# Kernel tuning notes

Hardware: AMD Instinct MI355X
Metric: run time of the kernel (lower is better)

## Reference

```python
import jax, jax.numpy as jnp
import numpy as np

HEADS = 16
DIM_HEAD = 64
SCALE = DIM_HEAD ** -0.5


def setup_inputs() -> dict:
    key = jax.random.key(0)
    ks = jax.random.split(key, 6)
    B, Nq, Nkv, D = 2, 512, 4096, 1024
    inner = HEADS * DIM_HEAD  # 1024
    s = 1.0 / np.sqrt(D)
    return {
        "q": jax.random.normal(ks[0], (B, Nq, D), jnp.float32),
        "kv": jax.random.normal(ks[1], (B, Nkv, D), jnp.float32),
        "mask": jnp.ones((B, Nkv), dtype=bool),
        "Wq": jax.random.normal(ks[2], (D, inner), jnp.float32) * s,
        "Wkv": jax.random.normal(ks[3], (D, 2 * inner), jnp.float32) * s,
        "Wo": jax.random.normal(ks[4], (inner, D), jnp.float32) * (1.0 / np.sqrt(inner)),
        "bo": jnp.zeros((D,), jnp.float32),
    }


def reference(q, kv, mask, Wq, Wkv, Wo, bo):
    B, Nq, D = q.shape
    Nkv = kv.shape[1]
    h, dh = HEADS, DIM_HEAD
    # projections
    qh = (q @ Wq).reshape(B, Nq, h, dh).transpose(0, 2, 1, 3)        # (B,h,Nq,dh)
    kvp = kv @ Wkv                                                    # (B,Nkv,2*inner)
    k, v = jnp.split(kvp, 2, axis=-1)
    kh = k.reshape(B, Nkv, h, dh).transpose(0, 2, 1, 3)              # (B,h,Nkv,dh)
    vh = v.reshape(B, Nkv, h, dh).transpose(0, 2, 1, 3)
    # scaled dot-product cross-attention
    attn = jnp.einsum("bhqd,bhkd->bhqk", qh, kh) * SCALE             # (B,h,Nq,Nkv)
    neg_inf = jnp.finfo(attn.dtype).min
    attn = jnp.where(mask[:, None, None, :], attn, neg_inf)
    attn = jax.nn.softmax(attn, axis=-1)
    out = jnp.einsum("bhqk,bhkd->bhqd", attn, vh)                    # (B,h,Nq,dh)
    out = out.transpose(0, 2, 1, 3).reshape(B, Nq, h * dh)
    return out @ Wo + bo
```

## Files before the change

### kernel.cpp

```cpp
#include <hip/hip_runtime.h>
#include <string.h>
#include <math.h>

typedef unsigned short u16;
typedef __bf16 bf16x8 __attribute__((ext_vector_type(8)));
typedef float floatx4 __attribute__((ext_vector_type(4)));

#define HEADS  16
#define DH     64
#define BATCH  2
#define NQ     512
#define NKV    4096
#define DMODEL 1024
#define INNER  1024
#define SCALE  0.125f
#define LOG2E  1.4426950408889634f
#define FM     12.0f
#define SPLIT  4
#define KEYS_PER_PART (NKV / SPLIT)
#define CH (KEYS_PER_PART / 64)

__device__ __forceinline__ u16 f2bf(float f) {
  union { __bf16 h; u16 u; } v; v.h = (__bf16)f; return v.u;
}

__device__ __forceinline__ void gll16(const u16* g, u16* l) {
  __builtin_amdgcn_global_load_lds(
      (const __attribute__((address_space(1))) unsigned int*)g,
      (__attribute__((address_space(3))) unsigned int*)l, 16, 0, 0);
}

__global__ __launch_bounds__(256) void prep(const float* __restrict__ q,
                                            const float* __restrict__ kv,
                                            const float* __restrict__ Wq,
                                            const float* __restrict__ Wkv,
                                            const float* __restrict__ Wo,
                                            u16* __restrict__ qb,
                                            u16* __restrict__ kvb,
                                            u16* __restrict__ Wqt,
                                            u16* __restrict__ Wkvt,
                                            u16* __restrict__ Wot) {
  __shared__ float tile[32][33];
  const int bx = blockIdx.x, tid = threadIdx.x;
  if (bx < 4608) {
    const float* x; u16* y; size_t i;
    if (bx < 512) { x = q;  y = qb;  i = (size_t)bx * 256 + tid; }
    else          { x = kv; y = kvb; i = (size_t)(bx - 512) * 256 + tid; }
    const float4* p = (const float4*)x + i * 2;
    float4 a = p[0], b = p[1];
    union { u16 s[8]; uint4 v; } o;
    o.s[0] = f2bf(a.x); o.s[1] = f2bf(a.y); o.s[2] = f2bf(a.z); o.s[3] = f2bf(a.w);
    o.s[4] = f2bf(b.x); o.s[5] = f2bf(b.y); o.s[6] = f2bf(b.z); o.s[7] = f2bf(b.w);
    *(uint4*)(y + i * 8) = o.v;
    return;
  }
  const float* W; u16* Wt; int K, N, n0, k0, t;
  if (bx < 5632)      { t = bx - 4608; W = Wq;  Wt = Wqt;  K = 1024; N = 1024; n0 = (t & 31) * 32; k0 = (t >> 5) * 32; }
  else if (bx < 7680) { t = bx - 5632; W = Wkv; Wt = Wkvt; K = 1024; N = 2048; n0 = (t & 63) * 32; k0 = (t >> 6) * 32; }
  else                { t = bx - 7680; W = Wo;  Wt = Wot;  K = 1024; N = 1024; n0 = (t & 31) * 32; k0 = (t >> 5) * 32; }
  const int tx = tid & 31, ty = tid >> 5;
  for (int i = 0; i < 32; i += 8)
    tile[ty + i][tx] = W[(size_t)(k0 + ty + i) * N + n0 + tx];
  __syncthreads();
  for (int i = 0; i < 32; i += 8)
    Wt[(size_t)(n0 + ty + i) * K + k0 + tx] = f2bf(tile[tx][ty + i]);
}

__global__ __launch_bounds__(256) void gemm_kv(const u16* __restrict__ A,
                                               const u16* __restrict__ Bt,
                                               u16* __restrict__ Kb,
                                               u16* __restrict__ Vb) {
  const int K = DMODEL;
  __shared__ __align__(16) u16 As[128 * 32];
  __shared__ __align__(16) u16 Bs[128 * 32];
  const int tid  = threadIdx.x;
  const int lane = tid & 63, wave = tid >> 6;
  const int wr = wave >> 1, wc = wave & 1;
  const int l16 = lane & 15, quad = lane >> 4;
  const int bm = blockIdx.y, bn = blockIdx.x;
  const int r0 = tid >> 2;
  const int kb = (tid & 3) ^ ((tid >> 3) & 3);
  const u16* aP0 = A  + ((size_t)bm * 128 + r0)      * K + kb * 8;
  const u16* aP1 = A  + ((size_t)bm * 128 + r0 + 64) * K + kb * 8;
  const u16* bP0 = Bt + ((size_t)bn * 128 + r0)      * K + kb * 8;
  const u16* bP1 = Bt + ((size_t)bn * 128 + r0 + 64) * K + kb * 8;
  u16* ldsA0 = As + wave * 512;
  u16* ldsA1 = As + 2048 + wave * 512;
  u16* ldsB0 = Bs + wave * 512;
  u16* ldsB1 = Bs + 2048 + wave * 512;
  const int ko = ((quad ^ ((l16 >> 1) & 3)) << 3);

  floatx4 acc[4][4] = {};
  for (int k0 = 0; k0 < K; k0 += 32) {
    gll16(aP0 + k0, ldsA0);
    gll16(aP1 + k0, ldsA1);
    gll16(bP0 + k0, ldsB0);
    gll16(bP1 + k0, ldsB1);
    __syncthreads();
    bf16x8 af[4], bfr[4];
#pragma unroll
    for (int i = 0; i < 4; ++i)
      af[i] = *(const bf16x8*)&As[(wr * 64 + i * 16 + l16) * 32 + ko];
#pragma unroll
    for (int j = 0; j < 4; ++j)
      bfr[j] = *(const bf16x8*)&Bs[(wc * 64 + j * 16 + l16) * 32 + ko];
#pragma unroll
    for (int i = 0; i < 4; ++i)
#pragma unroll
      for (int j = 0; j < 4; ++j)
        acc[i][j] = __builtin_amdgcn_mfma_f32_16x16x32_bf16(af[i], bfr[j], acc[i][j], 0, 0, 0);
    __syncthreads();
  }
  u16* Cb = (bn < 8) ? Kb : Vb;
  const int colbase = ((bn < 8) ? bn : bn - 8) * 128;
#pragma unroll
  for (int i = 0; i < 4; ++i) {
    const int rowb = bm * 128 + wr * 64 + i * 16 + quad * 4;
#pragma unroll
    for (int j = 0; j < 4; ++j) {
      const int col = colbase + wc * 64 + j * 16 + l16;
#pragma unroll
      for (int r = 0; r < 4; ++r)
        Cb[(size_t)(rowb + r) * 1024 + col] = f2bf(acc[i][j][r]);
    }
  }
}

template<bool OUT_BF16>
__global__ __launch_bounds__(256) void gemm64(const u16* __restrict__ A,
                                              const u16* __restrict__ Bt,
                                              float* __restrict__ Cf,
                                              u16* __restrict__ Cb,
                                              const float* __restrict__ bias,
                                              int M, int N, int K) {
  __shared__ __align__(16) u16 As[64 * 64];
  __shared__ __align__(16) u16 Bs[64 * 64];
  const int tid = threadIdx.x;
  const int lane = tid & 63, wave = tid >> 6;
  const int wr = wave >> 1, wc = wave & 1;
  const int l16 = lane & 15, quad = lane >> 4;
  const int bm = blockIdx.y, bn = blockIdx.x;
  const int r0 = tid >> 3;
  const int kbs = (tid & 7) ^ (r0 & 7);
  const u16* aP0 = A  + ((size_t)bm * 64 + r0)      * K + kbs * 8;
  const u16* aP1 = A  + ((size_t)bm * 64 + r0 + 32) * K + kbs * 8;
  const u16* bP0 = Bt + ((size_t)bn * 64 + r0)      * K + kbs * 8;
  const u16* bP1 = Bt + ((size_t)bn * 64 + r0 + 32) * K + kbs * 8;
  u16* ldsA0 = As + wave * 512;
  u16* ldsA1 = As + 2048 + wave * 512;
  u16* ldsB0 = Bs + wave * 512;
  u16* ldsB1 = Bs + 2048 + wave * 512;

  floatx4 acc[2][2] = {};
  for (int k0 = 0; k0 < K; k0 += 64) {
    gll16(aP0 + k0, ldsA0);
    gll16(aP1 + k0, ldsA1);
    gll16(bP0 + k0, ldsB0);
    gll16(bP1 + k0, ldsB1);
    __syncthreads();
    bf16x8 af[2][2], bfr[2][2];
#pragma unroll
    for (int i = 0; i < 2; ++i)
#pragma unroll
      for (int kk = 0; kk < 2; ++kk)
        af[i][kk] = *(const bf16x8*)&As[(wr * 32 + i * 16 + l16) * 64 +
                                        (((kk * 4 + quad) ^ (l16 & 7)) << 3)];
#pragma unroll
    for (int j = 0; j < 2; ++j)
#pragma unroll
      for (int kk = 0; kk < 2; ++kk)
        bfr[j][kk] = *(const bf16x8*)&Bs[(wc * 32 + j * 16 + l16) * 64 +
                                         (((kk * 4 + quad) ^ (l16 & 7)) << 3)];
#pragma unroll
    for (int i = 0; i < 2; ++i)
#pragma unroll
      for (int j = 0; j < 2; ++j) {
        acc[i][j] = __builtin_amdgcn_mfma_f32_16x16x32_bf16(af[i][0], bfr[j][0], acc[i][j], 0, 0, 0);
        acc[i][j] = __builtin_amdgcn_mfma_f32_16x16x32_bf16(af[i][1], bfr[j][1], acc[i][j], 0, 0, 0);
      }
    __syncthreads();
  }
#pragma unroll
  for (int i = 0; i < 2; ++i) {
    const int rowb = bm * 64 + wr * 32 + i * 16 + quad * 4;
#pragma unroll
    for (int j = 0; j < 2; ++j) {
      const int col = bn * 64 + wc * 32 + j * 16 + l16;
#pragma unroll
      for (int r = 0; r < 4; ++r) {
        const size_t idx = (size_t)(rowb + r) * N + col;
        if (OUT_BF16) Cb[idx] = f2bf(acc[i][j][r]);
        else          Cf[idx] = acc[i][j][r] + bias[col];
      }
    }
  }
}

__global__ __launch_bounds__(256) void vtrans(const u16* __restrict__ Vb,
                                              u16* __restrict__ vT) {
  __shared__ u16 t[64 * 72];
  const int bx = blockIdx.x, tid = threadIdx.x;
  const int bh = bx >> 6, tb = bx & 63;
  const int b = bh >> 4, h = bh & 15;
  const int r = tid >> 2, cg = (tid & 3) * 16;
  const u16* src = Vb + ((size_t)(b * NKV + tb * 64 + r)) * 1024 + h * 64 + cg;
  *(uint4*)&t[r * 72 + cg]     = ((const uint4*)src)[0];
  *(uint4*)&t[r * 72 + cg + 8] = ((const uint4*)src)[1];
  __syncthreads();
  const int d = tid >> 2, tg = (tid & 3) * 16;
  union { u16 s[16]; uint4 v[2]; } o;
#pragma unroll
  for (int i = 0; i < 16; ++i) o.s[i] = t[(tg + i) * 72 + d];
  u16* dst = vT + ((size_t)(bh * 64 + d)) * NKV + tb * 64 + tg;
  *(uint4*)dst = o.v[0]; *(uint4*)(dst + 8) = o.v[1];
}

__global__ __launch_bounds__(256) void attn_part(const u16* __restrict__ Qh,
                                                 const u16* __restrict__ Kb,
                                                 const u16* __restrict__ vT,
                                                 const int* __restrict__ mask,
                                                 float* __restrict__ Opart,
                                                 float* __restrict__ Mst,
                                                 float* __restrict__ Lst) {
  __shared__ __align__(16) u16 Ks[64 * 64];
  __shared__ __align__(16) u16 Vs[2][64 * 64];
  __shared__ __align__(16) u16 QP[4608];
  __shared__ float Msk[64];
  const int tid = threadIdx.x;
  const int lane = tid & 63, w = tid >> 6;
  const int l16 = lane & 15, quad = lane >> 4;
  const int part = blockIdx.x & (SPLIT - 1);
  const int qt = (blockIdx.x >> 2) & 7;
  const int h  = (blockIdx.x >> 5) & 15;
  const int b  = blockIdx.x >> 9;
  const int rs = tid >> 2, d0 = (tid & 3) * 16;
  u16* Ps = QP + w * 1152;

  const int r8 = lane >> 3;
  const int kb8 = (lane & 7) ^ (r8 & 7);
  const int key00 = part * KEYS_PER_PART;
  const u16* kSrc = Kb + ((size_t)(b * NKV + key00 + w * 8 + r8)) * 1024 + h * DH + kb8 * 8;
  const u16* vSrc = vT + ((size_t)((b * 16 + h) * 64 + w * 8 + r8)) * NKV + key00 + kb8 * 8;
  u16* ldsK0 = Ks + w * 512;
  u16* ldsK1 = Ks + 2048 + w * 512;
  const int koA = (quad ^ (l16 & 7)) << 3;
  const int koB = ((quad + 4) ^ (l16 & 7)) << 3;

  bf16x8 bones;
  {
    union { u16 s[8]; bf16x8 v; } t1;
    const u16 o1 = (l16 == 0) ? (u16)0x3F80 : (u16)0;
#pragma unroll
    for (int i = 0; i < 8; ++i) t1.s[i] = o1;
    bones = t1.v;
  }

  {
    const uint4* p = (const uint4*)(Qh + ((size_t)(b * NQ + qt * 64 + rs)) * INNER + h * DH + d0);
    *(uint4*)&QP[rs * 72 + d0]     = p[0];
    *(uint4*)&QP[rs * 72 + d0 + 8] = p[1];
  }
  gll16(kSrc, ldsK0);
  gll16(kSrc + 32768, ldsK1);
  gll16(vSrc, Vs[0] + w * 512);
  gll16(vSrc + (size_t)32 * NKV, Vs[0] + 2048 + w * 512);
  float mk0 = 0.f;
  if (tid < 64) mk0 = (mask[(size_t)b * NKV + key00 + tid] != 0) ? -FM : -1e30f;
  __syncthreads();
  bf16x8 aq0 = *(const bf16x8*)&QP[(w * 16 + l16) * 72 + quad * 8];
  bf16x8 aq1 = *(const bf16x8*)&QP[(w * 16 + l16) * 72 + 32 + quad * 8];
  if (tid < 64) Msk[tid] = mk0;
  __syncthreads();

  floatx4 o[4] = {};
  floatx4 lacc = {0.f, 0.f, 0.f, 0.f};
  const float SC = SCALE * LOG2E;

  for (int c = 0; c < CH; ++c) {
    const u16* Vcur = Vs[c & 1];
#pragma unroll
    for (int nt = 0; nt < 4; ++nt) {
      bf16x8 b0 = *(const bf16x8*)&Ks[(nt * 16 + l16) * 64 + koA];
      bf16x8 b1 = *(const bf16x8*)&Ks[(nt * 16 + l16) * 64 + koB];
      floatx4 t = {0.f, 0.f, 0.f, 0.f};
      t = __builtin_amdgcn_mfma_f32_16x16x32_bf16(aq0, b0, t, 0, 0, 0);
      t = __builtin_amdgcn_mfma_f32_16x16x32_bf16(aq1, b1, t, 0, 0, 0);
      const float mk = Msk[nt * 16 + l16];
#pragma unroll
      for (int r = 0; r < 4; ++r)
        Ps[(quad * 4 + r) * 72 + nt * 16 + l16] = f2bf(exp2f(t[r] * SC + mk));
    }
    __syncthreads();
    if (c + 1 < CH) {
      gll16(kSrc + (size_t)(c + 1) * 65536, ldsK0);
      gll16(kSrc + (size_t)(c + 1) * 65536 + 32768, ldsK1);
      u16* vdst = Vs[(c + 1) & 1];
      gll16(vSrc + (c + 1) * 64, vdst + w * 512);
      gll16(vSrc + (c + 1) * 64 + (size_t)32 * NKV, vdst + 2048 + w * 512);
      if (tid < 64)
        Msk[tid] = (mask[(size_t)b * NKV + key00 + (c + 1) * 64 + tid] != 0) ? -FM : -1e30f;
    }
    bf16x8 ap0 = *(const bf16x8*)&Ps[l16 * 72 + quad * 8];
    bf16x8 ap1 = *(const bf16x8*)&Ps[l16 * 72 + 32 + quad * 8];
    lacc = __builtin_amdgcn_mfma_f32_16x16x32_bf16(ap0, bones, lacc, 0, 0, 0);
    lacc = __builtin_amdgcn_mfma_f32_16x16x32_bf16(ap1, bones, lacc, 0, 0, 0);
#pragma unroll
    for (int dt = 0; dt < 4; ++dt) {
      bf16x8 bv0 = *(const bf16x8*)&Vcur[(dt * 16 + l16) * 64 + koA];
      bf16x8 bv1 = *(const bf16x8*)&Vcur[(dt * 16 + l16) * 64 + koB];
      o[dt] = __builtin_amdgcn_mfma_f32_16x16x32_bf16(ap0, bv0, o[dt], 0, 0, 0);
      o[dt] = __builtin_amdgcn_mfma_f32_16x16x32_bf16(ap1, bv1, o[dt], 0, 0, 0);
    }
    __syncthreads();
  }
  const int pid = blockIdx.x;
#pragma unroll
  for (int r = 0; r < 4; ++r) {
    const int q = w * 16 + quad * 4 + r;
    if (l16 == 0) { Mst[pid * 64 + q] = FM; Lst[pid * 64 + q] = lacc[r]; }
#pragma unroll
    for (int dt = 0; dt < 4; ++dt)
      Opart[(size_t)pid * 4096 + q * 64 + dt * 16 + l16] = o[dt][r];
  }
}

__global__ __launch_bounds__(256) void attn_combine(const float* __restrict__ Opart,
                                                    const float* __restrict__ Mst,
                                                    const float* __restrict__ Lst,
                                                    u16* __restrict__ Out) {
  const int x = blockIdx.x;
  const int t = threadIdx.x;
  const int q = t >> 2, db = (t & 3) * 16;
  const int b = x >> 7, h = (x >> 3) & 15, qt = x & 7;
  float ms[SPLIT], ls[SPLIT];
#pragma unroll
  for (int s = 0; s < SPLIT; ++s) {
    ms[s] = Mst[(size_t)(x * SPLIT + s) * 64 + q];
    ls[s] = Lst[(size_t)(x * SPLIT + s) * 64 + q];
  }
  float M = fmaxf(fmaxf(ms[0], ms[1]), fmaxf(ms[2], ms[3]));
  float wgt[SPLIT], L = 0.f;
#pragma unroll
  for (int s = 0; s < SPLIT; ++s) { wgt[s] = exp2f(ms[s] - M); L += wgt[s] * ls[s]; }
  const float inv = 1.0f / L;
  float acc[16] = {};
#pragma unroll
  for (int s = 0; s < SPLIT; ++s) {
    const float4* p = (const float4*)&Opart[(size_t)(x * SPLIT + s) * 4096 + q * 64 + db];
    const float ws = wgt[s];
#pragma unroll
    for (int i = 0; i < 4; ++i) {
      float4 v = p[i];
      acc[i * 4 + 0] += ws * v.x; acc[i * 4 + 1] += ws * v.y;
      acc[i * 4 + 2] += ws * v.z; acc[i * 4 + 3] += ws * v.w;
    }
  }
  union { u16 s[16]; uint4 v[2]; } ou;
#pragma unroll
  for (int i = 0; i < 16; ++i) ou.s[i] = f2bf(acc[i] * inv);
  u16* dst = Out + ((size_t)(b * NQ + qt * 64 + q)) * INNER + h * DH + db;
  *(uint4*)dst = ou.v[0]; *(uint4*)(dst + 8) = ou.v[1];
}

extern "C" void kernel_launch(void* const* d_in, const int* in_sizes, int n_in,
                              void* d_out, int out_size, void* d_ws, size_t ws_size,
                              hipStream_t stream) {
  const float* q    = (const float*)d_in[0];
  const float* kv   = (const float*)d_in[1];
  const int*   mask = (const int*)d_in[2];
  const float* Wq   = (const float*)d_in[3];
  const float* Wkv  = (const float*)d_in[4];
  const float* Wo   = (const float*)d_in[5];
  const float* bo   = (const float*)d_in[6];
  float* out = (float*)d_out;

  char* ws = (char*)d_ws;
  u16*   qb    = (u16*)(ws);
  u16*   kvb   = (u16*)(ws + (2u << 20));
  float* Mst   = (float*)(ws);
  float* Lst   = (float*)(ws + (256u << 10));
  u16*   vT    = (u16*)(ws + (2u << 20));
  u16* Wqt  = (u16*)(ws + (18u << 20));
  u16* Wkvt = (u16*)(ws + (20u << 20));
  u16* Wot  = (u16*)(ws + (24u << 20));
  u16* qh   = (u16*)(ws + (26u << 20));
  u16* Kb   = (u16*)(ws + (28u << 20));
  u16* Vb   = (u16*)(ws + (44u << 20));
  float* Opart = (float*)(ws + (44u << 20));
  u16* attn = (u16*)(ws + (60u << 20));

  prep<<<dim3(8704), 256, 0, stream>>>(q, kv, Wq, Wkv, Wo, qb, kvb, Wqt, Wkvt, Wot);
  gemm64<true><<<dim3(INNER / 64, (BATCH * NQ) / 64), 256, 0, stream>>>(
      qb, Wqt, nullptr, qh, nullptr, BATCH * NQ, INNER, DMODEL);
  gemm_kv<<<dim3(16, 64), 256, 0, stream>>>(kvb, Wkvt, Kb, Vb);
  vtrans<<<dim3(BATCH * HEADS * (NKV / 64)), 256, 0, stream>>>(Vb, vT);
  attn_part<<<dim3(BATCH * HEADS * (NQ / 64) * SPLIT), 256, 0, stream>>>(
      qh, Kb, vT, mask, Opart, Mst, Lst);
  attn_combine<<<dim3(BATCH * HEADS * (NQ / 64)), 256, 0, stream>>>(Opart, Mst, Lst, attn);
  gemm64<false><<<dim3(DMODEL / 64, (BATCH * NQ) / 64), 256, 0, stream>>>(
      attn, Wot, out, nullptr, bo, BATCH * NQ, DMODEL, INNER);
}
```

Before: 226.5 us.

## Fuse V transpose into KV GEMM epilogue and deepen K tile to 64

The KV projection GEMM now writes V directly in transposed head-major layout from its epilogue, so the separate vtrans kernel and its extra read/write pass over V are gone. The GEMM main loop also loads 64-wide K slices per iteration with a new XOR swizzle, halving the number of barriers per block. Workspace buffers are rearranged so Opart and vT no longer overlap. The transposed stores are 8-byte scattered writes along the token axis, which may coalesce worse than the old row-major writes, and the larger LDS footprint may reduce occupancy.

```diff
diff --git a/kernel.cpp b/kernel.cpp
--- a/kernel.cpp
+++ b/kernel.cpp
@@ -69,59 +69,76 @@
 __global__ __launch_bounds__(256) void gemm_kv(const u16* __restrict__ A,
                                                const u16* __restrict__ Bt,
                                                u16* __restrict__ Kb,
-                                               u16* __restrict__ Vb) {
+                                               u16* __restrict__ vT) {
   const int K = DMODEL;
-  __shared__ __align__(16) u16 As[128 * 32];
-  __shared__ __align__(16) u16 Bs[128 * 32];
+  __shared__ __align__(16) u16 As[128 * 64];
+  __shared__ __align__(16) u16 Bs[128 * 64];
   const int tid  = threadIdx.x;
   const int lane = tid & 63, wave = tid >> 6;
   const int wr = wave >> 1, wc = wave & 1;
   const int l16 = lane & 15, quad = lane >> 4;
   const int bm = blockIdx.y, bn = blockIdx.x;
-  const int r0 = tid >> 2;
-  const int kb = (tid & 3) ^ ((tid >> 3) & 3);
-  const u16* aP0 = A  + ((size_t)bm * 128 + r0)      * K + kb * 8;
-  const u16* aP1 = A  + ((size_t)bm * 128 + r0 + 64) * K + kb * 8;
-  const u16* bP0 = Bt + ((size_t)bn * 128 + r0)      * K + kb * 8;
-  const u16* bP1 = Bt + ((size_t)bn * 128 + r0 + 64) * K + kb * 8;
-  u16* ldsA0 = As + wave * 512;
-  u16* ldsA1 = As + 2048 + wave * 512;
-  u16* ldsB0 = Bs + wave * 512;
-  u16* ldsB1 = Bs + 2048 + wave * 512;
-  const int ko = ((quad ^ ((l16 >> 1) & 3)) << 3);
+  const int r8 = lane >> 3;
+  const int kb8 = (lane & 7) ^ r8;
+  const u16* aP = A  + ((size_t)bm * 128 + wave * 8 + r8) * K + kb8 * 8;
+  const u16* bP = Bt + ((size_t)bn * 128 + wave * 8 + r8) * K + kb8 * 8;
 
   floatx4 acc[4][4] = {};
-  for (int k0 = 0; k0 < K; k0 += 32) {
-    gll16(aP0 + k0, ldsA0);
-    gll16(aP1 + k0, ldsA1);
-    gll16(bP0 + k0, ldsB0);
-    gll16(bP1 + k0, ldsB1);
-    __syncthreads();
-    bf16x8 af[4], bfr[4];
+  for (int k0 = 0; k0 < K; k0 += 64) {
+#pragma unroll
+    for (int p = 0; p < 4; ++p) {
+      gll16(aP + (size_t)p * 32 * K + k0, As + p * 2048 + wave * 512);
+      gll16(bP + (size_t)p * 32 * K + k0, Bs + p * 2048 + wave * 512);
+    }
+    __syncthreads();
+    bf16x8 af[4][2], bfr[4][2];
 #pragma unroll
     for (int i = 0; i < 4; ++i)
-      af[i] = *(const bf16x8*)&As[(wr * 64 + i * 16 + l16) * 32 + ko];
+#pragma unroll
+      for (int h2 = 0; h2 < 2; ++h2)
+        af[i][h2] = *(const bf16x8*)&As[(wr * 64 + i * 16 + l16) * 64 +
+                                        (((h2 * 4 + quad) ^ (l16 & 7)) << 3)];
 #pragma unroll
     for (int j = 0; j < 4; ++j)
-      bfr[j] = *(const bf16x8*)&Bs[(wc * 64 + j * 16 + l16) * 32 + ko];
+#pragma unroll
+      for (int h2 = 0; h2 < 2; ++h2)
+        bfr[j][h2] = *(const bf16x8*)&Bs[(wc * 64 + j * 16 + l16) * 64 +
+                                         (((h2 * 4 + quad) ^ (l16 & 7)) << 3)];
 #pragma unroll
     for (int i = 0; i < 4; ++i)
 #pragma unroll
-      for (int j = 0; j < 4; ++j)
-        acc[i][j] = __builtin_amdgcn_mfma_f32_16x16x32_bf16(af[i], bfr[j], acc[i][j], 0, 0, 0);
-    __syncthreads();
-  }
-  u16* Cb = (bn < 8) ? Kb : Vb;
-  const int colbase = ((bn < 8) ? bn : bn - 8) * 128;
-#pragma unroll
-  for (int i = 0; i < 4; ++i) {
-    const int rowb = bm * 128 + wr * 64 + i * 16 + quad * 4;
-#pragma unroll
-    for (int j = 0; j < 4; ++j) {
-      const int col = colbase + wc * 64 + j * 16 + l16;
-#pragma unroll
-      for (int r = 0; r < 4; ++r)
-        Cb[(size_t)(rowb + r) * 1024 + col] = f2bf(acc[i][j][r]);
+      for (int j = 0; j < 4; ++j) {
+        acc[i][j] = __builtin_amdgcn_mfma_f32_16x16x32_bf16(af[i][0], bfr[j][0], acc[i][j], 0, 0, 0);
+        acc[i][j] = __builtin_amdgcn_mfma_f32_16x16x32_bf16(af[i][1], bfr[j][1], acc[i][j], 0, 0, 0);
+      }
+    __syncthreads();
+  }
+  if (bn < 8) {
+#pragma unroll
+    for (int i = 0; i < 4; ++i) {
+      const int rowb = bm * 128 + wr * 64 + i * 16 + quad * 4;
+#pragma unroll
+      for (int j = 0; j < 4; ++j) {
+        const int col = bn * 128 + wc * 64 + j * 16 + l16;
+#pragma unroll
+        for (int r = 0; r < 4; ++r)
+          Kb[(size_t)(rowb + r) * 1024 + col] = f2bf(acc[i][j][r]);
+      }
+    }
+  } else {
+    const int b = bm >> 5;
+    const int tokb = (bm & 31) * 128;
+#pragma unroll
+    for (int i = 0; i < 4; ++i) {
+      const int tok0 = tokb + wr * 64 + i * 16 + quad * 4;
+#pragma unroll
+      for (int j = 0; j < 4; ++j) {
+        const int d = (bn - 8) * 128 + wc * 64 + j * 16 + l16;
+        union { u16 s[4]; uint2 v; } pk;
+#pragma unroll
+        for (int r = 0; r < 4; ++r) pk.s[r] = f2bf(acc[i][j][r]);
+        *(uint2*)(vT + ((size_t)(b * 1024 + d)) * NKV + tok0) = pk.v;
+      }
     }
   }
 }
@@ -196,25 +213,6 @@
   }
 }
 
-__global__ __launch_bounds__(256) void vtrans(const u16* __restrict__ Vb,
-                                              u16* __restrict__ vT) {
-  __shared__ u16 t[64 * 72];
-  const int bx = blockIdx.x, tid = threadIdx.x;
-  const int bh = bx >> 6, tb = bx & 63;
-  const int b = bh >> 4, h = bh & 15;
-  const int r = tid >> 2, cg = (tid & 3) * 16;
-  const u16* src = Vb + ((size_t)(b * NKV + tb * 64 + r)) * 1024 + h * 64 + cg;
-  *(uint4*)&t[r * 72 + cg]     = ((const uint4*)src)[0];
-  *(uint4*)&t[r * 72 + cg + 8] = ((const uint4*)src)[1];
-  __syncthreads();
-  const int d = tid >> 2, tg = (tid & 3) * 16;
-  union { u16 s[16]; uint4 v[2]; } o;
-#pragma unroll
-  for (int i = 0; i < 16; ++i) o.s[i] = t[(tg + i) * 72 + d];
-  u16* dst = vT + ((size_t)(bh * 64 + d)) * NKV + tb * 64 + tg;
-  *(uint4*)dst = o.v[0]; *(uint4*)(dst + 8) = o.v[1];
-}
-
 __global__ __launch_bounds__(256) void attn_part(const u16* __restrict__ Qh,
                                                  const u16* __restrict__ Kb,
                                                  const u16* __restrict__ vT,
@@ -379,21 +377,19 @@
   u16*   kvb   = (u16*)(ws + (2u << 20));
   float* Mst   = (float*)(ws);
   float* Lst   = (float*)(ws + (256u << 10));
-  u16*   vT    = (u16*)(ws + (2u << 20));
+  float* Opart = (float*)(ws + (2u << 20));
   u16* Wqt  = (u16*)(ws + (18u << 20));
   u16* Wkvt = (u16*)(ws + (20u << 20));
   u16* Wot  = (u16*)(ws + (24u << 20));
   u16* qh   = (u16*)(ws + (26u << 20));
   u16* Kb   = (u16*)(ws + (28u << 20));
-  u16* Vb   = (u16*)(ws + (44u << 20));
-  float* Opart = (float*)(ws + (44u << 20));
+  u16* vT   = (u16*)(ws + (44u << 20));
   u16* attn = (u16*)(ws + (60u << 20));
 
   prep<<<dim3(8704), 256, 0, stream>>>(q, kv, Wq, Wkv, Wo, qb, kvb, Wqt, Wkvt, Wot);
   gemm64<true><<<dim3(INNER / 64, (BATCH * NQ) / 64), 256, 0, stream>>>(
       qb, Wqt, nullptr, qh, nullptr, BATCH * NQ, INNER, DMODEL);
-  gemm_kv<<<dim3(16, 64), 256, 0, stream>>>(kvb, Wkvt, Kb, Vb);
-  vtrans<<<dim3(BATCH * HEADS * (NKV / 64)), 256, 0, stream>>>(Vb, vT);
+  gemm_kv<<<dim3(16, 64), 256, 0, stream>>>(kvb, Wkvt, Kb, vT);
   attn_part<<<dim3(BATCH * HEADS * (NQ / 64) * SPLIT), 256, 0, stream>>>(
       qh, Kb, vT, mask, Opart, Mst, Lst);
   attn_combine<<<dim3(BATCH * HEADS * (NQ / 64)), 256, 0, stream>>>(Opart, Mst, Lst, attn);
```

After: 213.4 us. 1.06x faster.
